# Optimization experiments

Measured on AMD Instinct MI355X. Metric: run time of the kernel, lower is better.

Reference implementation:

```python
import jax, jax.numpy as jnp
import numpy as np

B, S, D = 4, 2048, 1024
H = 16
DH = D // H          # 64
DFF = 4096
EPS = 1e-5


def _layer_norm(x, gamma, beta):
    mu = jnp.mean(x, axis=-1, keepdims=True)
    var = jnp.mean(jnp.square(x - mu), axis=-1, keepdims=True)
    return (x - mu) * jax.lax.rsqrt(var + EPS) * gamma + beta


def setup_inputs() -> dict:
    key = jax.random.key(0)
    ks = jax.random.split(key, 8)
    s_in = 1.0 / np.sqrt(D)
    s_ff = 1.0 / np.sqrt(DFF)
    return {
        "x": jax.random.normal(ks[0], (B, S, D), dtype=jnp.float32),
        # per-head qkv weights stacked: [H, D, 3*DH] (nn.Linear, bias=False)
        "Wqkv": jax.random.normal(ks[1], (H, D, 3 * DH), dtype=jnp.float32) * s_in,
        "Wproj": jax.random.normal(ks[2], (D, D), dtype=jnp.float32) * s_in,
        "bproj": jnp.zeros((D,), dtype=jnp.float32),
        "ln1_g": jnp.ones((D,), dtype=jnp.float32),
        "ln1_b": jnp.zeros((D,), dtype=jnp.float32),
        "ln2_g": jnp.ones((D,), dtype=jnp.float32),
        "ln2_b": jnp.zeros((D,), dtype=jnp.float32),
        "W1": jax.random.normal(ks[3], (D, DFF), dtype=jnp.float32) * s_in,
        "b1": jnp.zeros((DFF,), dtype=jnp.float32),
        "W2": jax.random.normal(ks[4], (DFF, D), dtype=jnp.float32) * s_ff,
        "b2": jnp.zeros((D,), dtype=jnp.float32),
    }


def reference(x, Wqkv, Wproj, bproj, ln1_g, ln1_b, ln2_g, ln2_b, W1, b1, W2, b2):
    # fused multi-head QKV projection: [B,S,D] x [H,D,3*DH] -> [B,H,S,3*DH]
    qkv = jnp.einsum('bsd,hde->bhse', x, Wqkv)
    q, k, v = jnp.split(qkv, 3, axis=-1)          # each [B,H,S,DH]
    scale = 1.0 / jnp.sqrt(jnp.asarray(DH, dtype=x.dtype))
    scores = jnp.einsum('bhsd,bhtd->bhst', q, k) * scale   # [B,H,S,S]
    causal = jnp.tril(jnp.ones((S, S), dtype=bool))
    scores = jnp.where(causal, scores, jnp.finfo(x.dtype).min)
    attn = jax.nn.softmax(scores, axis=-1)
    heads = jnp.einsum('bhst,bhtd->bhsd', attn, v)          # [B,H,S,DH]
    att_out = heads.transpose(0, 2, 1, 3).reshape(B, S, D)  # concat heads
    att_out = att_out @ Wproj + bproj
    out = _layer_norm(x + att_out, ln1_g, ln1_b)            # dropout = identity (eval)
    mlp_out = (jax.nn.gelu(out @ W1 + b1, approximate=False)) @ W2 + b2
    out = _layer_norm(out + mlp_out, ln2_g, ln2_b)
    return out
```

## Files before the change

### kernel.cpp

```cpp
#include <hip/hip_runtime.h>
#include <math.h>

#define BB 4
#define SS 2048
#define DD 1024
#define HH 16
#define DHH 64
#define DFF 4096
static constexpr float LN_EPS = 1e-5f;

typedef __bf16 bf16x8 __attribute__((ext_vector_type(8)));
typedef float f32x4 __attribute__((ext_vector_type(4)));
typedef unsigned short u16x8 __attribute__((ext_vector_type(8)));

__device__ inline unsigned short f2bf(float f) {
    union { float f; unsigned int u; } v; v.f = f;
    unsigned int u = v.u + 0x7FFFu + ((v.u >> 16) & 1u);
    return (unsigned short)(u >> 16);
}

__device__ __forceinline__ float fexp2(float x) {
    return __builtin_amdgcn_exp2f(x);
}

__device__ __forceinline__ void gl_lds16(const unsigned short* g,
                                         unsigned short* l) {
    __builtin_amdgcn_global_load_lds(
        (const __attribute__((address_space(1))) unsigned int*)g,
        (__attribute__((address_space(3))) unsigned int*)l, 16, 0, 0);
}

#define GBAR()                               \
    do {                                     \
        asm volatile("" ::: "memory");       \
        __builtin_amdgcn_s_barrier();        \
        asm volatile("" ::: "memory");       \
    } while (0)
#define VMCNT(n) asm volatile("s_waitcnt vmcnt(" #n ")" ::: "memory")

__global__ __launch_bounds__(256) void transpose_bf16_kernel(
    const float* __restrict__ in, unsigned short* __restrict__ outT,
    int R, int C) {
    __shared__ float t[64][65];
    const int r0 = blockIdx.y * 64, c0 = blockIdx.x * 64;
    const int cl = threadIdx.x & 63, rl = threadIdx.x >> 6;
#pragma unroll
    for (int rr = 0; rr < 16; ++rr)
        t[rl + rr * 4][cl] = in[(size_t)(r0 + rl + rr * 4) * C + c0 + cl];
    __syncthreads();
#pragma unroll
    for (int rr = 0; rr < 16; ++rr)
        outT[(size_t)(c0 + rl + rr * 4) * R + r0 + cl] = f2bf(t[cl][rl + rr * 4]);
}

__global__ __launch_bounds__(256) void repack_wqkv_bf16_kernel(
    const float* __restrict__ Wqkv, unsigned short* __restrict__ Wq2T) {
    __shared__ float t[64][65];
    const int h = blockIdx.z;
    const int d0 = blockIdx.y * 64, e0 = blockIdx.x * 64;
    const int cl = threadIdx.x & 63, rl = threadIdx.x >> 6;
#pragma unroll
    for (int rr = 0; rr < 16; ++rr)
        t[rl + rr * 4][cl] =
            Wqkv[((size_t)h * DD + d0 + rl + rr * 4) * 192 + e0 + cl];
    __syncthreads();
#pragma unroll
    for (int rr = 0; rr < 16; ++rr)
        Wq2T[((size_t)h * 192 + e0 + rl + rr * 4) * DD + d0 + cl] =
            f2bf(t[cl][rl + rr * 4]);
}

__global__ __launch_bounds__(256) void f2bf_kernel(
    const float* __restrict__ in, unsigned short* __restrict__ out, int n) {
    int i = blockIdx.x * 256 + threadIdx.x;
    if (i < n) out[i] = f2bf(in[i]);
}

__device__ __forceinline__ void read_afrag(const unsigned short* s, int base,
                                           int wm, int l15, int g,
                                           bf16x8 af[4][2]) {
#pragma unroll
    for (int ii = 0; ii < 4; ++ii) {
        const int lr = wm * 64 + ii * 16 + l15;
#pragma unroll
        for (int ks = 0; ks < 2; ++ks) {
            const int p = ((ks << 2) + g) ^ (lr & 7);
            af[ii][ks] = __builtin_bit_cast(
                bf16x8, *(const u16x8*)&s[base + lr * 64 + p * 8]);
        }
    }
}

__device__ __forceinline__ void read_bfrag(const unsigned short* s, int base,
                                           int wn, int l15, int g,
                                           bf16x8 bf2[2][2]) {
#pragma unroll
    for (int jj = 0; jj < 2; ++jj) {
        const int lr = wn * 32 + jj * 16 + l15;
#pragma unroll
        for (int ks = 0; ks < 2; ++ks) {
            const int p = ((ks << 2) + g) ^ (lr & 7);
            bf2[jj][ks] = __builtin_bit_cast(
                bf16x8, *(const u16x8*)&s[base + lr * 64 + p * 8]);
        }
    }
}

template <int RS>
__device__ __forceinline__ void stage_half(const unsigned short* __restrict__ G,
                                           int ldK, int growbase, int kbase,
                                           unsigned short* lbase, int tid) {
#pragma unroll
    for (int s = 0; s < 2; ++s) {
        const int c16 = s * 512 + tid;
        const int r = c16 >> 3, c = c16 & 7;
        const int grow =
            growbase + ((r >> RS) << (RS + 1)) + (r & ((1 << RS) - 1));
        const int gcol = kbase + ((c ^ (r & 7)) << 3);
        gl_lds16(&G[(size_t)grow * ldK + gcol], &lbase[c16 << 3]);
    }
}

template <int MH, int NH>
__device__ __forceinline__ void mfma_quad(f32x4 acc[8][4],
                                          const bf16x8 af[4][2],
                                          const bf16x8 bf2[2][2]) {
    __builtin_amdgcn_s_setprio(1);
#pragma unroll
    for (int ks = 0; ks < 2; ++ks)
#pragma unroll
        for (int ii = 0; ii < 4; ++ii)
#pragma unroll
            for (int jj = 0; jj < 2; ++jj)
                acc[MH * 4 + ii][NH * 2 + jj] =
                    __builtin_amdgcn_mfma_f32_16x16x32_bf16(
                        af[ii][ks], bf2[jj][ks],
                        acc[MH * 4 + ii][NH * 2 + jj], 0, 0, 0);
    __builtin_amdgcn_s_setprio(0);
}

template <int MODE>
__global__ __launch_bounds__(512) void mfma_gemm256_kernel(
    const unsigned short* __restrict__ A, const unsigned short* __restrict__ BT,
    float* __restrict__ Cf, unsigned short* __restrict__ Cb,
    const float* __restrict__ bias, const float* __restrict__ resid,
    unsigned short* __restrict__ Qb, unsigned short* __restrict__ Kb,
    unsigned short* __restrict__ VTb, int M, int N, int K) {
    __shared__ __align__(16) unsigned short smem[65536];
    const int tid = threadIdx.x;
    const int lane = tid & 63, wave = tid >> 6;
    const int wm = wave >> 2, wn = wave & 3;
    const int l15 = lane & 15, g = lane >> 4;

    const int gx = gridDim.x, nwg = gx * gridDim.y;
    const int lid = blockIdx.y * gx + blockIdx.x;
    const int swz = ((nwg & 7) == 0) ? ((lid & 7) * (nwg >> 3) + (lid >> 3))
                                     : lid;
    const int row0 = (swz / gx) * 256;
    const int col0 = (swz % gx) * 256;

    const int kt = K >> 6;

    f32x4 acc[8][4] = {};

    stage_half<6>(A, K, row0, 0, smem + 0, tid);
    stage_half<6>(A, K, row0 + 64, 0, smem + 8192, tid);
    stage_half<5>(BT, K, col0, 0, smem + 32768, tid);
    stage_half<5>(BT, K, col0 + 32, 0, smem + 40960, tid);
    VMCNT(4);
    stage_half<6>(A, K, row0, 64, smem + 16384, tid);
    stage_half<6>(A, K, row0 + 64, 64, smem + 24576, tid);
    stage_half<5>(BT, K, col0, 64, smem + 49152, tid);
    VMCNT(6);
    GBAR();

    bf16x8 af[4][2], bf0[2][2], bf1[2][2];
    for (int it = 0; it < (kt >> 1); ++it) {
        const int t1k = (2 * it + 1) << 6;
        int t2 = 2 * it + 2; if (t2 > kt - 1) t2 = kt - 1;
        int t3 = 2 * it + 3; if (t3 > kt - 1) t3 = kt - 1;
        const int t2k = t2 << 6, t3k = t3 << 6;

        read_afrag(smem, 0, wm, l15, g, af);
        read_bfrag(smem, 32768, wn, l15, g, bf0);
        stage_half<5>(BT, K, col0 + 32, t1k, smem + 57344, tid);
        GBAR();
        mfma_quad<0, 0>(acc, af, bf0);
        GBAR();

        read_bfrag(smem, 40960, wn, l15, g, bf1);
        stage_half<6>(A, K, row0, t2k, smem + 0, tid);
        GBAR();
        mfma_quad<0, 1>(acc, af, bf1);
        GBAR();

        read_afrag(smem, 8192, wm, l15, g, af);
        stage_half<5>(BT, K, col0, t2k, smem + 32768, tid);
        GBAR();
        mfma_quad<1, 1>(acc, af, bf1);
        GBAR();

        stage_half<6>(A, K, row0 + 64, t2k, smem + 8192, tid);
        GBAR();
        mfma_quad<1, 0>(acc, af, bf0);
        VMCNT(6);
        GBAR();

        read_afrag(smem, 16384, wm, l15, g, af);
        read_bfrag(smem, 49152, wn, l15, g, bf0);
        stage_half<5>(BT, K, col0 + 32, t2k, smem + 40960, tid);
        GBAR();
        mfma_quad<0, 0>(acc, af, bf0);
        GBAR();

        read_bfrag(smem, 57344, wn, l15, g, bf1);
        stage_half<6>(A, K, row0, t3k, smem + 16384, tid);
        GBAR();
        mfma_quad<0, 1>(acc, af, bf1);
        GBAR();

        read_afrag(smem, 24576, wm, l15, g, af);
        stage_half<5>(BT, K, col0, t3k, smem + 49152, tid);
        GBAR();
        mfma_quad<1, 1>(acc, af, bf1);
        GBAR();

        stage_half<6>(A, K, row0 + 64, t3k, smem + 24576, tid);
        GBAR();
        mfma_quad<1, 0>(acc, af, bf0);
        VMCNT(6);
        GBAR();
    }
    VMCNT(0);
    GBAR();

    if (MODE == 2) {
        constexpr int SLAB = 264;
#pragma unroll
        for (int i2 = 0; i2 < 8; ++i2) {
            __syncthreads();
#pragma unroll
            for (int j2 = 0; j2 < 4; ++j2) {
                const int col = wn * 64 + j2 * 16 + l15;
                const float bv = bias[col0 + col];
#pragma unroll
                for (int r = 0; r < 4; ++r) {
                    float v = acc[i2][j2][r] + bv;
                    float t = fexp2(v * (2.30211849f + 0.10294198f * v * v));
                    float gel = v * t * __builtin_amdgcn_rcpf(t + 1.f);
                    smem[(wm * 16 + g * 4 + r) * SLAB + col] = f2bf(gel);
                }
            }
            __syncthreads();
            const int sr = tid >> 4;
            const int cc = (tid & 15) * 16;
            const int grow = row0 + ((sr >> 4) << 7) + i2 * 16 + (sr & 15);
            *(u16x8*)&Cb[(size_t)grow * N + col0 + cc] =
                *(const u16x8*)&smem[sr * SLAB + cc];
            *(u16x8*)&Cb[(size_t)grow * N + col0 + cc + 8] =
                *(const u16x8*)&smem[sr * SLAB + cc + 8];
        }
        return;
    }

#pragma unroll
    for (int i2 = 0; i2 < 8; ++i2) {
#pragma unroll
        for (int j2 = 0; j2 < 4; ++j2) {
            const int col = col0 + wn * 64 + j2 * 16 + l15;
            const int rowb = row0 + wm * 128 + i2 * 16 + g * 4;
            if (MODE == 4) {
                const int h = col / 192, e = col % 192;
                const int bb = rowb >> 11, s = rowb & 2047;
                if (e < 64) {
                    unsigned short* q =
                        Qb + (((size_t)bb * HH + h) * SS + s) * 64 + e;
#pragma unroll
                    for (int r = 0; r < 4; ++r)
                        q[r * 64] = f2bf(acc[i2][j2][r] * 0.18033688f);
                } else if (e < 128) {
                    unsigned short* kp =
                        Kb + (((size_t)bb * HH + h) * SS + s) * 64 + (e - 64);
#pragma unroll
                    for (int r = 0; r < 4; ++r)
                        kp[r * 64] = f2bf(acc[i2][j2][r]);
                } else {
                    ushort4 pk;
                    pk.x = f2bf(acc[i2][j2][0]);
                    pk.y = f2bf(acc[i2][j2][1]);
                    pk.z = f2bf(acc[i2][j2][2]);
                    pk.w = f2bf(acc[i2][j2][3]);
                    *(ushort4*)(VTb + (((size_t)bb * HH + h) * 64 + (e - 128)) *
                                          SS + s) = pk;
                }
            } else {
                const float bv = bias[col];
#pragma unroll
                for (int r = 0; r < 4; ++r) {
                    const int row = rowb + r;
                    float v = acc[i2][j2][r] + bv + resid[(size_t)row * N + col];
                    Cf[(size_t)row * N + col] = v;
                }
            }
        }
    }
}

__global__ __launch_bounds__(256) void fattn_kernel(
    const unsigned short* __restrict__ Qb, const unsigned short* __restrict__ Kb,
    const unsigned short* __restrict__ VTb, unsigned short* __restrict__ att) {
    constexpr int QSTR = 68, KSTR = 68, VSTR = 76, PSTR = 68;
    __shared__ __align__(16) unsigned short Pls[128 * PSTR];
    __shared__ __align__(16) unsigned short Kls[64 * KSTR];
    __shared__ __align__(16) unsigned short VTls[64 * VSTR];

    const int bh = blockIdx.x;
    const int q0 = blockIdx.y * 128;
    const int tid = threadIdx.x;
    const int lane = tid & 63;
    const int wave = tid >> 6;
    const int l15 = lane & 15;
    const int g = lane >> 4;
    const int b = bh >> 4, h = bh & 15;

    const unsigned short* Qh = Qb + (size_t)bh * SS * 64;
    const unsigned short* Kh = Kb + (size_t)bh * SS * 64;
    const unsigned short* Vh = VTb + (size_t)bh * 64 * SS;

    {
        const int row = tid >> 1, c0 = (tid & 1) * 32;
        const unsigned short* src = Qh + (size_t)(q0 + row) * 64 + c0;
        unsigned short* dst = &Pls[row * QSTR + c0];
#pragma unroll
        for (int c = 0; c < 32; c += 8)
            *(u16x8*)(dst + c) = *(const u16x8*)(src + c);
    }
    __syncthreads();
    bf16x8 qf[2][2];
#pragma unroll
    for (int i = 0; i < 2; ++i)
#pragma unroll
        for (int ks = 0; ks < 2; ++ks)
            qf[i][ks] = __builtin_bit_cast(
                bf16x8, *(const u16x8*)&Pls[(wave * 32 + i * 16 + l15) * QSTR +
                                            ks * 32 + g * 8]);
    __syncthreads();

    f32x4 oacc[4][2] = {};
    float mst[2], lst[2];
#pragma unroll
    for (int i = 0; i < 2; ++i) { mst[i] = -1e30f; lst[i] = 0.f; }

    const int srow = tid >> 2, sc0 = (tid & 3) * 16;
    const int qlim = q0 + wave * 32 + 31;
    const int qrow = wave * 32 + l15;

    for (int t0 = 0; t0 <= q0 + 64; t0 += 64) {
        __syncthreads();
        {
            const unsigned short* ksrc = Kh + (size_t)(t0 + srow) * 64 + sc0;
            *(u16x8*)&Kls[srow * KSTR + sc0]     = *(const u16x8*)ksrc;
            *(u16x8*)&Kls[srow * KSTR + sc0 + 8] = *(const u16x8*)(ksrc + 8);
            const unsigned short* vsrc = Vh + (size_t)srow * SS + t0 + sc0;
            *(u16x8*)&VTls[srow * VSTR + sc0]     = *(const u16x8*)vsrc;
            *(u16x8*)&VTls[srow * VSTR + sc0 + 8] = *(const u16x8*)(vsrc + 8);
        }
        __syncthreads();
        if (t0 > qlim) continue;

        f32x4 sacc[4][2] = {};
#pragma unroll
        for (int ks = 0; ks < 2; ++ks) {
            bf16x8 kb[4];
#pragma unroll
            for (int j = 0; j < 4; ++j)
                kb[j] = __builtin_bit_cast(
                    bf16x8, *(const u16x8*)&Kls[(j * 16 + l15) * KSTR +
                                                ks * 32 + g * 8]);
#pragma unroll
            for (int j = 0; j < 4; ++j)
#pragma unroll
                for (int i = 0; i < 2; ++i)
                    sacc[j][i] = __builtin_amdgcn_mfma_f32_16x16x32_bf16(
                        kb[j], qf[i][ks], sacc[j][i], 0, 0, 0);
        }

        if (t0 >= q0) {
#pragma unroll
            for (int j = 0; j < 4; ++j)
#pragma unroll
                for (int i = 0; i < 2; ++i)
#pragma unroll
                    for (int r = 0; r < 4; ++r) {
                        const int kg = t0 + j * 16 + g * 4 + r;
                        const int qg = q0 + qrow + i * 16;
                        if (kg > qg) sacc[j][i][r] = -1e30f;
                    }
        }

#pragma unroll
        for (int i = 0; i < 2; ++i) {
            float mx = -1e30f;
#pragma unroll
            for (int j = 0; j < 4; ++j)
#pragma unroll
                for (int r = 0; r < 4; ++r) mx = fmaxf(mx, sacc[j][i][r]);
            mx = fmaxf(mx, __shfl_xor(mx, 16));
            mx = fmaxf(mx, __shfl_xor(mx, 32));
            const float mn = fmaxf(mst[i], mx);
            const float al = fexp2(mst[i] - mn);
            mst[i] = mn;
            float rsum = 0.f;
            const int pbase = (qrow + i * 16) * PSTR + g * 4;
#pragma unroll
            for (int j = 0; j < 4; ++j) {
                float p0 = fexp2(sacc[j][i][0] - mn);
                float p1 = fexp2(sacc[j][i][1] - mn);
                float p2 = fexp2(sacc[j][i][2] - mn);
                float p3 = fexp2(sacc[j][i][3] - mn);
                rsum += (p0 + p1) + (p2 + p3);
                ushort4 pk;
                pk.x = f2bf(p0); pk.y = f2bf(p1);
                pk.z = f2bf(p2); pk.w = f2bf(p3);
                *(ushort4*)&Pls[pbase + j * 16] = pk;
            }
            rsum += __shfl_xor(rsum, 16);
            rsum += __shfl_xor(rsum, 32);
            lst[i] = lst[i] * al + rsum;
#pragma unroll
            for (int jo = 0; jo < 4; ++jo)
#pragma unroll
                for (int r = 0; r < 4; ++r) oacc[jo][i][r] *= al;
        }
        __syncthreads();

#pragma unroll
        for (int ks = 0; ks < 2; ++ks) {
            bf16x8 vb[4], pf[2];
#pragma unroll
            for (int jo = 0; jo < 4; ++jo)
                vb[jo] = __builtin_bit_cast(
                    bf16x8, *(const u16x8*)&VTls[(jo * 16 + l15) * VSTR +
                                                 ks * 32 + g * 8]);
#pragma unroll
            for (int i = 0; i < 2; ++i)
                pf[i] = __builtin_bit_cast(
                    bf16x8, *(const u16x8*)&Pls[(qrow + i * 16) * PSTR +
                                                ks * 32 + g * 8]);
#pragma unroll
            for (int jo = 0; jo < 4; ++jo)
#pragma unroll
                for (int i = 0; i < 2; ++i)
                    oacc[jo][i] = __builtin_amdgcn_mfma_f32_16x16x32_bf16(
                        vb[jo], pf[i], oacc[jo][i], 0, 0, 0);
        }
    }

#pragma unroll
    for (int i = 0; i < 2; ++i) {
        const float inv = 1.f / lst[i];
        const int qg = q0 + qrow + i * 16;
        unsigned short* dst = att + ((size_t)b * SS + qg) * DD + h * 64 + g * 4;
#pragma unroll
        for (int jo = 0; jo < 4; ++jo) {
            ushort4 pk;
            pk.x = f2bf(oacc[jo][i][0] * inv);
            pk.y = f2bf(oacc[jo][i][1] * inv);
            pk.z = f2bf(oacc[jo][i][2] * inv);
            pk.w = f2bf(oacc[jo][i][3] * inv);
            *(ushort4*)(dst + jo * 16) = pk;
        }
    }
}

__global__ __launch_bounds__(256) void ln_kernel(
    const float* __restrict__ X, const float* __restrict__ g,
    const float* __restrict__ bta, float* __restrict__ Y,
    unsigned short* __restrict__ Yb) {
    const int row = blockIdx.x;
    const float4 xv = ((const float4*)(X + (size_t)row * DD))[threadIdx.x];

    __shared__ float red1[4], red2[4];
    float s = xv.x + xv.y + xv.z + xv.w;
#pragma unroll
    for (int off = 32; off > 0; off >>= 1) s += __shfl_down(s, off);
    const int wave = threadIdx.x >> 6;
    if ((threadIdx.x & 63) == 0) red1[wave] = s;
    __syncthreads();
    const float mu = (red1[0] + red1[1] + red1[2] + red1[3]) * (1.f / DD);

    float dx = xv.x - mu, dy = xv.y - mu, dz = xv.z - mu, dw = xv.w - mu;
    float s2 = dx * dx + dy * dy + dz * dz + dw * dw;
#pragma unroll
    for (int off = 32; off > 0; off >>= 1) s2 += __shfl_down(s2, off);
    if ((threadIdx.x & 63) == 0) red2[wave] = s2;
    __syncthreads();
    const float var = (red2[0] + red2[1] + red2[2] + red2[3]) * (1.f / DD);
    const float rstd = rsqrtf(var + LN_EPS);

    const float4 gv = ((const float4*)g)[threadIdx.x];
    const float4 bv = ((const float4*)bta)[threadIdx.x];
    float4 yv;
    yv.x = dx * rstd * gv.x + bv.x;
    yv.y = dy * rstd * gv.y + bv.y;
    yv.z = dz * rstd * gv.z + bv.z;
    yv.w = dw * rstd * gv.w + bv.w;
    ((float4*)(Y + (size_t)row * DD))[threadIdx.x] = yv;
    if (Yb) {
        ushort4 q;
        q.x = f2bf(yv.x); q.y = f2bf(yv.y);
        q.z = f2bf(yv.z); q.w = f2bf(yv.w);
        ((ushort4*)(Yb + (size_t)row * DD))[threadIdx.x] = q;
    }
}

extern "C" void kernel_launch(void* const* d_in, const int* in_sizes, int n_in,
                              void* d_out, int out_size, void* d_ws,
                              size_t ws_size, hipStream_t stream) {
    const float* x     = (const float*)d_in[0];
    const float* Wqkv  = (const float*)d_in[1];
    const float* Wproj = (const float*)d_in[2];
    const float* bproj = (const float*)d_in[3];
    const float* ln1_g = (const float*)d_in[4];
    const float* ln1_b = (const float*)d_in[5];
    const float* ln2_g = (const float*)d_in[6];
    const float* ln2_b = (const float*)d_in[7];
    const float* W1    = (const float*)d_in[8];
    const float* b1    = (const float*)d_in[9];
    const float* W2    = (const float*)d_in[10];
    const float* b2    = (const float*)d_in[11];
    float* out = (float*)d_out;

    const size_t M = (size_t)BB * SS;
    const size_t MB = 1024 * 1024;
    char* w = (char*)d_ws;
    unsigned short* Qb     = (unsigned short*)(w + 0);
    unsigned short* out1b  = (unsigned short*)(w + 0);
    unsigned short* Kb     = (unsigned short*)(w + 16 * MB);
    unsigned short* VTb    = (unsigned short*)(w + 32 * MB);
    unsigned short* hbuf   = (unsigned short*)(w + 16 * MB);
    unsigned short* Wq2T   = (unsigned short*)(w + 96 * MB);
    unsigned short* xb     = (unsigned short*)(w + 102 * MB);
    unsigned short* att    = (unsigned short*)(w + 96 * MB);
    float*          out1   = (float*)(w + 96 * MB);
    unsigned short* WprojT = (unsigned short*)(w + 118 * MB);
    unsigned short* W1T    = (unsigned short*)(w + 128 * MB);
    unsigned short* W2T    = (unsigned short*)(w + 136 * MB);

    repack_wqkv_bf16_kernel<<<dim3(3, 16, 16), 256, 0, stream>>>(Wqkv, Wq2T);
    transpose_bf16_kernel<<<dim3(16, 16), 256, 0, stream>>>(Wproj, WprojT, 1024, 1024);
    transpose_bf16_kernel<<<dim3(64, 16), 256, 0, stream>>>(W1, W1T, 1024, 4096);
    transpose_bf16_kernel<<<dim3(16, 64), 256, 0, stream>>>(W2, W2T, 4096, 1024);
    f2bf_kernel<<<(int)((M * DD + 255) / 256), 256, 0, stream>>>(x, xb, (int)(M * DD));

    mfma_gemm256_kernel<4><<<dim3(3072 / 256, M / 256), 512, 0, stream>>>(
        xb, Wq2T, nullptr, nullptr, nullptr, nullptr, Qb, Kb, VTb,
        (int)M, 3072, 1024);

    fattn_kernel<<<dim3(BB * HH, SS / 128), 256, 0, stream>>>(Qb, Kb, VTb, att);

    mfma_gemm256_kernel<3><<<dim3(1024 / 256, M / 256), 512, 0, stream>>>(
        att, WprojT, out, nullptr, bproj, x, nullptr, nullptr, nullptr,
        (int)M, 1024, 1024);

    ln_kernel<<<(int)M, 256, 0, stream>>>(out, ln1_g, ln1_b, out1, out1b);

    mfma_gemm256_kernel<2><<<dim3(4096 / 256, M / 256), 512, 0, stream>>>(
        out1b, W1T, nullptr, hbuf, b1, nullptr, nullptr, nullptr, nullptr,
        (int)M, 4096, 1024);

    mfma_gemm256_kernel<3><<<dim3(1024 / 256, M / 256), 512, 0, stream>>>(
        hbuf, W2T, out, nullptr, b2, out1, nullptr, nullptr, nullptr,
        (int)M, 1024, 4096);

    ln_kernel<<<(int)M, 256, 0, stream>>>(out, ln2_g, ln2_b, out, nullptr);
}
```

Baseline: 553.9 us.

## Add 256x128-tile GEMM kernel for QKV, projection and FFN-down GEMMs

Introduces a gemm_n128 kernel with 256x128 output tiles, its own staging/fragment helpers and pipelined k-loop, and uses it for the QKV, output projection and W2 GEMMs. For N=1024 the 256x256 tiling launched only 128 workgroups, underfilling the GPU; halving the N tile doubles the workgroup count to improve CU occupancy and wave balance. The trade-off is lower per-tile data reuse and more A-matrix re-reads from memory.

```diff
diff --git a/kernel.cpp b/kernel.cpp
--- a/kernel.cpp
+++ b/kernel.cpp
@@ -76,36 +76,6 @@
     if (i < n) out[i] = f2bf(in[i]);
 }
 
-__device__ __forceinline__ void read_afrag(const unsigned short* s, int base,
-                                           int wm, int l15, int g,
-                                           bf16x8 af[4][2]) {
-#pragma unroll
-    for (int ii = 0; ii < 4; ++ii) {
-        const int lr = wm * 64 + ii * 16 + l15;
-#pragma unroll
-        for (int ks = 0; ks < 2; ++ks) {
-            const int p = ((ks << 2) + g) ^ (lr & 7);
-            af[ii][ks] = __builtin_bit_cast(
-                bf16x8, *(const u16x8*)&s[base + lr * 64 + p * 8]);
-        }
-    }
-}
-
-__device__ __forceinline__ void read_bfrag(const unsigned short* s, int base,
-                                           int wn, int l15, int g,
-                                           bf16x8 bf2[2][2]) {
-#pragma unroll
-    for (int jj = 0; jj < 2; ++jj) {
-        const int lr = wn * 32 + jj * 16 + l15;
-#pragma unroll
-        for (int ks = 0; ks < 2; ++ks) {
-            const int p = ((ks << 2) + g) ^ (lr & 7);
-            bf2[jj][ks] = __builtin_bit_cast(
-                bf16x8, *(const u16x8*)&s[base + lr * 64 + p * 8]);
-        }
-    }
-}
-
 template <int RS>
 __device__ __forceinline__ void stage_half(const unsigned short* __restrict__ G,
                                            int ldK, int growbase, int kbase,
@@ -121,6 +91,45 @@
     }
 }
 
+__device__ __forceinline__ void stage_64(const unsigned short* __restrict__ G,
+                                         int ldK, int growbase, int kbase,
+                                         unsigned short* lbase, int tid) {
+    const int r = tid >> 3, c = tid & 7;
+    const int grow = growbase + ((r >> 5) << 6) + (r & 31);
+    const int gcol = kbase + ((c ^ (r & 7)) << 3);
+    gl_lds16(&G[(size_t)grow * ldK + gcol], &lbase[tid << 3]);
+}
+
+__device__ __forceinline__ void read_afrag(const unsigned short* s, int base,
+                                           int wm, int l15, int g,
+                                           bf16x8 af[4][2]) {
+#pragma unroll
+    for (int ii = 0; ii < 4; ++ii) {
+        const int lr = wm * 64 + ii * 16 + l15;
+#pragma unroll
+        for (int ks = 0; ks < 2; ++ks) {
+            const int p = ((ks << 2) + g) ^ (lr & 7);
+            af[ii][ks] = __builtin_bit_cast(
+                bf16x8, *(const u16x8*)&s[base + lr * 64 + p * 8]);
+        }
+    }
+}
+
+__device__ __forceinline__ void read_bfrag(const unsigned short* s, int base,
+                                           int wn, int l15, int g,
+                                           bf16x8 bf2[2][2]) {
+#pragma unroll
+    for (int jj = 0; jj < 2; ++jj) {
+        const int lr = wn * 32 + jj * 16 + l15;
+#pragma unroll
+        for (int ks = 0; ks < 2; ++ks) {
+            const int p = ((ks << 2) + g) ^ (lr & 7);
+            bf2[jj][ks] = __builtin_bit_cast(
+                bf16x8, *(const u16x8*)&s[base + lr * 64 + p * 8]);
+        }
+    }
+}
+
 template <int MH, int NH>
 __device__ __forceinline__ void mfma_quad(f32x4 acc[8][4],
                                           const bf16x8 af[4][2],
@@ -144,8 +153,7 @@
     const unsigned short* __restrict__ A, const unsigned short* __restrict__ BT,
     float* __restrict__ Cf, unsigned short* __restrict__ Cb,
     const float* __restrict__ bias, const float* __restrict__ resid,
-    unsigned short* __restrict__ Qb, unsigned short* __restrict__ Kb,
-    unsigned short* __restrict__ VTb, int M, int N, int K) {
+    int M, int N, int K) {
     __shared__ __align__(16) unsigned short smem[65536];
     const int tid = threadIdx.x;
     const int lane = tid & 63, wave = tid >> 6;
@@ -269,6 +277,166 @@
         for (int j2 = 0; j2 < 4; ++j2) {
             const int col = col0 + wn * 64 + j2 * 16 + l15;
             const int rowb = row0 + wm * 128 + i2 * 16 + g * 4;
+            const float bv = bias[col];
+#pragma unroll
+            for (int r = 0; r < 4; ++r) {
+                const int row = rowb + r;
+                float v = acc[i2][j2][r] + bv + resid[(size_t)row * N + col];
+                Cf[(size_t)row * N + col] = v;
+            }
+        }
+    }
+}
+
+__device__ __forceinline__ void read_af128(const unsigned short* s, int base,
+                                           int wm, int l15, int g,
+                                           bf16x8 af[2][2]) {
+#pragma unroll
+    for (int ii = 0; ii < 2; ++ii) {
+        const int lr = wm * 32 + ii * 16 + l15;
+#pragma unroll
+        for (int ks = 0; ks < 2; ++ks) {
+            const int p = ((ks << 2) + g) ^ (lr & 7);
+            af[ii][ks] = __builtin_bit_cast(
+                bf16x8, *(const u16x8*)&s[base + lr * 64 + p * 8]);
+        }
+    }
+}
+
+__device__ __forceinline__ void read_bf128(const unsigned short* s, int base,
+                                           int wn, int l15, int g,
+                                           bf16x8 bf2[2][2]) {
+#pragma unroll
+    for (int jj = 0; jj < 2; ++jj) {
+        const int lr = wn * 32 + jj * 16 + l15;
+#pragma unroll
+        for (int ks = 0; ks < 2; ++ks) {
+            const int p = ((ks << 2) + g) ^ (lr & 7);
+            bf2[jj][ks] = __builtin_bit_cast(
+                bf16x8, *(const u16x8*)&s[base + lr * 64 + p * 8]);
+        }
+    }
+}
+
+template <int MH, int NH>
+__device__ __forceinline__ void mfma_quad128(f32x4 acc[4][4],
+                                             const bf16x8 af[2][2],
+                                             const bf16x8 bf2[2][2]) {
+    __builtin_amdgcn_s_setprio(1);
+#pragma unroll
+    for (int ks = 0; ks < 2; ++ks)
+#pragma unroll
+        for (int ii = 0; ii < 2; ++ii)
+#pragma unroll
+            for (int jj = 0; jj < 2; ++jj)
+                acc[MH * 2 + ii][NH * 2 + jj] =
+                    __builtin_amdgcn_mfma_f32_16x16x32_bf16(
+                        af[ii][ks], bf2[jj][ks],
+                        acc[MH * 2 + ii][NH * 2 + jj], 0, 0, 0);
+    __builtin_amdgcn_s_setprio(0);
+}
+
+template <int MODE>
+__global__ __launch_bounds__(512) void gemm_n128_kernel(
+    const unsigned short* __restrict__ A, const unsigned short* __restrict__ BT,
+    float* __restrict__ Cf, const float* __restrict__ bias,
+    const float* __restrict__ resid, unsigned short* __restrict__ Qb,
+    unsigned short* __restrict__ Kb, unsigned short* __restrict__ VTb,
+    int M, int N, int K) {
+    __shared__ __align__(16) unsigned short smem[49152];
+    const int tid = threadIdx.x;
+    const int lane = tid & 63, wave = tid >> 6;
+    const int wm = wave >> 1, wn = wave & 1;
+    const int l15 = lane & 15, g = lane >> 4;
+
+    const int gx = gridDim.x, nwg = gx * gridDim.y;
+    const int lid = blockIdx.y * gx + blockIdx.x;
+    const int swz = ((nwg & 7) == 0) ? ((lid & 7) * (nwg >> 3) + (lid >> 3))
+                                     : lid;
+    const int row0 = (swz / gx) * 256;
+    const int col0 = (swz % gx) * 128;
+
+    const int kt = K >> 6;
+
+    f32x4 acc[4][4] = {};
+
+    stage_half<5>(A, K, row0, 0, smem + 0, tid);
+    stage_half<5>(A, K, row0 + 32, 0, smem + 8192, tid);
+    stage_64(BT, K, col0, 0, smem + 32768, tid);
+    stage_64(BT, K, col0 + 32, 0, smem + 36864, tid);
+    VMCNT(4);
+    stage_half<5>(A, K, row0, 64, smem + 16384, tid);
+    stage_half<5>(A, K, row0 + 32, 64, smem + 24576, tid);
+    stage_64(BT, K, col0, 64, smem + 40960, tid);
+    VMCNT(5);
+    GBAR();
+
+    bf16x8 af[2][2], bf0[2][2], bf1[2][2];
+    for (int it = 0; it < (kt >> 1); ++it) {
+        const int t1k = (2 * it + 1) << 6;
+        int t2 = 2 * it + 2; if (t2 > kt - 1) t2 = kt - 1;
+        int t3 = 2 * it + 3; if (t3 > kt - 1) t3 = kt - 1;
+        const int t2k = t2 << 6, t3k = t3 << 6;
+
+        read_af128(smem, 0, wm, l15, g, af);
+        read_bf128(smem, 32768, wn, l15, g, bf0);
+        stage_64(BT, K, col0 + 32, t1k, smem + 45056, tid);
+        GBAR();
+        mfma_quad128<0, 0>(acc, af, bf0);
+        GBAR();
+
+        read_bf128(smem, 36864, wn, l15, g, bf1);
+        stage_half<5>(A, K, row0, t2k, smem + 0, tid);
+        GBAR();
+        mfma_quad128<0, 1>(acc, af, bf1);
+        GBAR();
+
+        read_af128(smem, 8192, wm, l15, g, af);
+        stage_64(BT, K, col0, t2k, smem + 32768, tid);
+        GBAR();
+        mfma_quad128<1, 1>(acc, af, bf1);
+        GBAR();
+
+        stage_half<5>(A, K, row0 + 32, t2k, smem + 8192, tid);
+        GBAR();
+        mfma_quad128<1, 0>(acc, af, bf0);
+        VMCNT(5);
+        GBAR();
+
+        read_af128(smem, 16384, wm, l15, g, af);
+        read_bf128(smem, 40960, wn, l15, g, bf0);
+        stage_64(BT, K, col0 + 32, t2k, smem + 36864, tid);
+        GBAR();
+        mfma_quad128<0, 0>(acc, af, bf0);
+        GBAR();
+
+        read_bf128(smem, 45056, wn, l15, g, bf1);
+        stage_half<5>(A, K, row0, t3k, smem + 16384, tid);
+        GBAR();
+        mfma_quad128<0, 1>(acc, af, bf1);
+        GBAR();
+
+        read_af128(smem, 24576, wm, l15, g, af);
+        stage_64(BT, K, col0, t3k, smem + 40960, tid);
+        GBAR();
+        mfma_quad128<1, 1>(acc, af, bf1);
+        GBAR();
+
+        stage_half<5>(A, K, row0 + 32, t3k, smem + 24576, tid);
+        GBAR();
+        mfma_quad128<1, 0>(acc, af, bf0);
+        VMCNT(5);
+        GBAR();
+    }
+    VMCNT(0);
+    GBAR();
+
+#pragma unroll
+    for (int i2 = 0; i2 < 4; ++i2) {
+#pragma unroll
+        for (int j2 = 0; j2 < 4; ++j2) {
+            const int col = col0 + wn * 64 + j2 * 16 + l15;
+            const int rowb = row0 + wm * 64 + i2 * 16 + g * 4;
             if (MODE == 4) {
                 const int h = col / 192, e = col % 192;
                 const int bb = rowb >> 11, s = rowb & 2047;
@@ -553,24 +721,22 @@
     transpose_bf16_kernel<<<dim3(16, 64), 256, 0, stream>>>(W2, W2T, 4096, 1024);
     f2bf_kernel<<<(int)((M * DD + 255) / 256), 256, 0, stream>>>(x, xb, (int)(M * DD));
 
-    mfma_gemm256_kernel<4><<<dim3(3072 / 256, M / 256), 512, 0, stream>>>(
-        xb, Wq2T, nullptr, nullptr, nullptr, nullptr, Qb, Kb, VTb,
-        (int)M, 3072, 1024);
+    gemm_n128_kernel<4><<<dim3(3072 / 128, M / 256), 512, 0, stream>>>(
+        xb, Wq2T, nullptr, nullptr, nullptr, Qb, Kb, VTb, (int)M, 3072, 1024);
 
     fattn_kernel<<<dim3(BB * HH, SS / 128), 256, 0, stream>>>(Qb, Kb, VTb, att);
 
-    mfma_gemm256_kernel<3><<<dim3(1024 / 256, M / 256), 512, 0, stream>>>(
-        att, WprojT, out, nullptr, bproj, x, nullptr, nullptr, nullptr,
+    gemm_n128_kernel<3><<<dim3(1024 / 128, M / 256), 512, 0, stream>>>(
+        att, WprojT, out, bproj, x, nullptr, nullptr, nullptr,
         (int)M, 1024, 1024);
 
     ln_kernel<<<(int)M, 256, 0, stream>>>(out, ln1_g, ln1_b, out1, out1b);
 
     mfma_gemm256_kernel<2><<<dim3(4096 / 256, M / 256), 512, 0, stream>>>(
-        out1b, W1T, nullptr, hbuf, b1, nullptr, nullptr, nullptr, nullptr,
-        (int)M, 4096, 1024);
-
-    mfma_gemm256_kernel<3><<<dim3(1024 / 256, M / 256), 512, 0, stream>>>(
-        hbuf, W2T, out, nullptr, b2, out1, nullptr, nullptr, nullptr,
+        out1b, W1T, nullptr, hbuf, b1, nullptr, (int)M, 4096, 1024);
+
+    gemm_n128_kernel<3><<<dim3(1024 / 128, M / 256), 512, 0, stream>>>(
+        hbuf, W2T, out, b2, out1, nullptr, nullptr, nullptr,
         (int)M, 1024, 4096);
 
     ln_kernel<<<(int)M, 256, 0, stream>>>(out, ln2_g, ln2_b, out, nullptr);
```

New measurement: 510.3 us. 7.9% less time.
